# Performance work log

Hardware: AMD Instinct MI355X
Metric: run time of the kernel (lower is better)

The kernel has to match this reference:

```python
import jax, jax.numpy as jnp
import numpy as np
from math import sqrt

B, S, D_MODEL = 2, 2048, 1024
H = 16
ADIM = D_MODEL // H  # 64
K_REL = 16
N_PEMB = 2 * K_REL + 1  # 33, bidirectional rel-pos vocabulary


def setup_inputs() -> dict:
    key = jax.random.key(0)
    ks = jax.random.split(key, 8)
    sc = 0.02
    return {
        "iQ": jax.random.normal(ks[0], (B, S, D_MODEL), jnp.float32),
        "iK": jax.random.normal(ks[1], (B, S, D_MODEL), jnp.float32),
        "iV": jax.random.normal(ks[2], (B, S, D_MODEL), jnp.float32),
        "Wq": jax.random.normal(ks[3], (D_MODEL, D_MODEL), jnp.float32) * sc,
        "Wk": jax.random.normal(ks[4], (D_MODEL, D_MODEL), jnp.float32) * sc,
        "Wv": jax.random.normal(ks[5], (D_MODEL, D_MODEL), jnp.float32) * sc,
        "Wo": jax.random.normal(ks[6], (D_MODEL, D_MODEL), jnp.float32) * sc,
        "rel_pemb": jax.random.normal(ks[7], (N_PEMB, ADIM), jnp.float32) * sc,
    }


def reference(iQ, iK, iV, Wq, Wk, Wv, Wo, rel_pemb):
    b, nq, _ = iQ.shape
    seql = iK.shape[1]
    # projections -> [b, h, len, d]
    q = (iQ @ Wq).reshape(b, nq, H, ADIM).transpose(0, 2, 1, 3)
    k = (iK @ Wk).reshape(b, seql, H, ADIM).transpose(0, 2, 1, 3)
    v = (iV @ Wv).reshape(b, seql, H, ADIM).transpose(0, 2, 1, 3)
    # content scores: [b, h, nq, seql]
    scores = jnp.einsum("bhqd,bhsd->bhqs", q, k)
    # relative position bias: rel[i, j] = clamp(j - i, -K, K) + K
    pos = jnp.arange(seql)
    rel = jnp.clip(pos[None, :] - pos[:, None], -K_REL, K_REL) + K_REL
    rel = rel[seql - nq:, :]  # narrow to query rows: [nq, seql]
    e = rel_pemb[rel]  # [nq, seql, d]
    scores = scores + jnp.einsum("bhqd,qsd->bhqs", q, e)
    scores = scores / sqrt(ADIM)
    attn = jax.nn.softmax(scores, axis=-1)
    ctx = jnp.einsum("bhqs,bhsd->bqhd", attn, v).reshape(b, nq, H * ADIM)
    return ctx @ Wo
```

## Files before the change

kernel.cpp:

```cpp
#include <hip/hip_runtime.h>
#include <hip/hip_bf16.h>

#define BB 2
#define S 2048
#define DM 1024
#define H 16
#define ADIM 64
#define NP 33

typedef __bf16 bf16x8 __attribute__((ext_vector_type(8)));
typedef float f32x4 __attribute__((ext_vector_type(4)));

__global__ __launch_bounds__(256) void wtrans(
    const float* __restrict__ W0, const float* __restrict__ W1,
    const float* __restrict__ W2, __bf16* __restrict__ T0,
    __bf16* __restrict__ T1, __bf16* __restrict__ T2) {
  const float* W; __bf16* T;
  switch (blockIdx.z) {
    case 0: W = W0; T = T0; break;
    case 1: W = W1; T = T1; break;
    default: W = W2; T = T2; break;
  }
  __shared__ __bf16 tile[64][65];
  int j = threadIdx.x & 63, i0 = threadIdx.x >> 6;
  int n0 = blockIdx.x * 64, k0 = blockIdx.y * 64;
#pragma unroll
  for (int p = 0; p < 16; ++p) {
    int i = i0 + p * 4;
    tile[i][j] = (__bf16)W[(size_t)(k0 + i) * DM + n0 + j];
  }
  __syncthreads();
#pragma unroll
  for (int p = 0; p < 16; ++p) {
    int i = i0 + p * 4;
    T[(size_t)(n0 + i) * DM + k0 + j] = tile[j][i];
  }
}

#define LDK 40
template <bool A_FP32, typename CT>
__device__ __forceinline__ void gemm_body(const void* __restrict__ Av,
                                          const __bf16* __restrict__ BT,
                                          CT* __restrict__ C, int mode) {
  __shared__ __bf16 As[128 * LDK];
  __shared__ __bf16 Bs[128 * LDK];
  int t = threadIdx.x;
  int w = t >> 6, lane = t & 63, l15 = lane & 15, quad = lane >> 4;
  int wm = w >> 1, wn = w & 1;
  int m0 = blockIdx.y * 128, n0 = blockIdx.x * 128;
  f32x4 acc[4][4] = {};
  int lr = t >> 2;
  int lk = (t & 3) * 8;
  for (int k0 = 0; k0 < DM; k0 += 32) {
#pragma unroll
    for (int rr = 0; rr < 2; ++rr) {
      int row = rr * 64 + lr;
      if constexpr (A_FP32) {
        const float* src = (const float*)Av + (size_t)(m0 + row) * DM + k0 + lk;
        float4 a0 = *(const float4*)src;
        float4 a1 = *(const float4*)(src + 4);
        bf16x8 v;
        v[0] = (__bf16)a0.x; v[1] = (__bf16)a0.y;
        v[2] = (__bf16)a0.z; v[3] = (__bf16)a0.w;
        v[4] = (__bf16)a1.x; v[5] = (__bf16)a1.y;
        v[6] = (__bf16)a1.z; v[7] = (__bf16)a1.w;
        *(bf16x8*)&As[row * LDK + lk] = v;
      } else {
        *(bf16x8*)&As[row * LDK + lk] =
            *(const bf16x8*)((const __bf16*)Av + (size_t)(m0 + row) * DM + k0 + lk);
      }
      *(bf16x8*)&Bs[row * LDK + lk] =
          *(const bf16x8*)&BT[(size_t)(n0 + row) * DM + k0 + lk];
    }
    __syncthreads();
    bf16x8 af[4], bfr[4];
#pragma unroll
    for (int mi = 0; mi < 4; ++mi)
      af[mi] = *(const bf16x8*)&As[(wm * 64 + mi * 16 + l15) * LDK + quad * 8];
#pragma unroll
    for (int ni = 0; ni < 4; ++ni)
      bfr[ni] = *(const bf16x8*)&Bs[(wn * 64 + ni * 16 + l15) * LDK + quad * 8];
#pragma unroll
    for (int mi = 0; mi < 4; ++mi)
#pragma unroll
      for (int ni = 0; ni < 4; ++ni)
        acc[mi][ni] = __builtin_amdgcn_mfma_f32_16x16x32_bf16(
            af[mi], bfr[ni], acc[mi][ni], 0, 0, 0);
    __syncthreads();
  }
#pragma unroll
  for (int mi = 0; mi < 4; ++mi)
#pragma unroll
    for (int ni = 0; ni < 4; ++ni)
#pragma unroll
      for (int r = 0; r < 4; ++r) {
        int row = m0 + wm * 64 + mi * 16 + quad * 4 + r;
        int col = n0 + wn * 64 + ni * 16 + l15;
        CT v = (CT)acc[mi][ni][r];
        if (mode == 0) {
          C[(size_t)row * DM + col] = v;
        } else {
          int b = row >> 11, s = row & (S - 1);
          int h = col >> 6, d = col & (ADIM - 1);
          if (mode == 1)
            C[((size_t)(b * H + h) * S + s) * ADIM + d] = v;
          else
            C[((size_t)(b * H + h) * ADIM + d) * S + s] = v;
        }
      }
}

__global__ __launch_bounds__(256) void proj3(
    const float* __restrict__ iQ, const float* __restrict__ iK,
    const float* __restrict__ iV, const __bf16* __restrict__ WqT,
    const __bf16* __restrict__ WkT, const __bf16* __restrict__ WvT,
    __bf16* __restrict__ Qw, __bf16* __restrict__ Kw,
    __bf16* __restrict__ Vt) {
  const float* A; const __bf16* B; __bf16* C; int mode;
  switch (blockIdx.z) {
    case 0: A = iQ; B = WqT; C = Qw; mode = 1; break;
    case 1: A = iK; B = WkT; C = Kw; mode = 1; break;
    default: A = iV; B = WvT; C = Vt; mode = 2; break;
  }
  gemm_body<true, __bf16>(A, B, C, mode);
}

__global__ __launch_bounds__(256) void gemm_final(
    const __bf16* __restrict__ ctx, const __bf16* __restrict__ WoT,
    float* __restrict__ out) {
  gemm_body<false, float>(ctx, WoT, out, 0);
}

#define AST 72
__global__ __launch_bounds__(256) void attn_flash(
    const __bf16* __restrict__ Qw, const __bf16* __restrict__ Kw,
    const __bf16* __restrict__ Vt, const float* __restrict__ pemb,
    __bf16* __restrict__ ctx) {
  int bh = blockIdx.y, b = bh >> 4, h = bh & 15;
  int q0 = blockIdx.x * 64;
  int t = threadIdx.x, w = t >> 6, lane = t & 63, l15 = lane & 15,
      quad = lane >> 4;
  const __bf16* Qh = Qw + (size_t)bh * S * ADIM;
  const __bf16* Kh = Kw + (size_t)bh * S * ADIM;
  const __bf16* Vh = Vt + (size_t)bh * ADIM * S;

  __shared__ __align__(16) char smem[36352];
  __bf16* Ks = (__bf16*)smem;
  __bf16* Vs = (__bf16*)(smem + 9216);
  float* pband = (float*)(smem + 18432);
  __bf16* pbufw = (__bf16*)(smem + 27136 + w * 2304);
  __bf16* peb = (__bf16*)smem;

  for (int i = t; i < 48 * 64; i += 256) {
    int r = i >> 6, d = i & 63;
    peb[r * AST + d] = (r < NP) ? (__bf16)pemb[i] : (__bf16)0.f;
  }

  int qa = q0 + w * 16 + l15;
  bf16x8 qf0 = *(const bf16x8*)&Qh[(size_t)qa * ADIM + quad * 8];
  bf16x8 qf1 = *(const bf16x8*)&Qh[(size_t)qa * ADIM + 32 + quad * 8];
  __syncthreads();

  {
    f32x4 pc[3] = {};
#pragma unroll
    for (int ni = 0; ni < 3; ++ni) {
      bf16x8 b0 = *(const bf16x8*)&peb[(ni * 16 + l15) * AST + quad * 8];
      bf16x8 b1 = *(const bf16x8*)&peb[(ni * 16 + l15) * AST + 32 + quad * 8];
      pc[ni] = __builtin_amdgcn_mfma_f32_16x16x32_bf16(qf0, b0, pc[ni], 0, 0, 0);
      pc[ni] = __builtin_amdgcn_mfma_f32_16x16x32_bf16(qf1, b1, pc[ni], 0, 0, 0);
    }
#pragma unroll
    for (int ni = 0; ni < 3; ++ni)
#pragma unroll
      for (int r = 0; r < 4; ++r) {
        int col = ni * 16 + l15;
        if (col < NP) pband[(w * 16 + quad * 4 + r) * 34 + col] = pc[ni][r];
      }
  }
  __syncthreads();

  int qc = q0 + w * 16 + quad * 4;
  int lrow = w * 16 + quad * 4;
  int qw0 = q0 + w * 16;
  float lsum[4] = {0.f, 0.f, 0.f, 0.f};
  f32x4 o[4] = {};

  float blo[4], bhi[4];
#pragma unroll
  for (int r = 0; r < 4; ++r) {
    blo[r] = __expf(pband[(lrow + r) * 34 + 0] * 0.125f);
    bhi[r] = __expf(pband[(lrow + r) * 34 + 32] * 0.125f);
  }

  int srow = t >> 3;
  int scol = (t & 7) * 8;
  bf16x8 k0r = *(const bf16x8*)&Kh[(size_t)srow * ADIM + scol];
  bf16x8 k1r = *(const bf16x8*)&Kh[(size_t)(32 + srow) * ADIM + scol];
  bf16x8 v0r = *(const bf16x8*)&Vh[(size_t)srow * S + scol];
  bf16x8 v1r = *(const bf16x8*)&Vh[(size_t)(32 + srow) * S + scol];

  for (int s0 = 0; s0 < S; s0 += 64) {
    __syncthreads();
    *(bf16x8*)&Ks[srow * AST + scol] = k0r;
    *(bf16x8*)&Ks[(32 + srow) * AST + scol] = k1r;
    *(bf16x8*)&Vs[srow * AST + scol] = v0r;
    *(bf16x8*)&Vs[(32 + srow) * AST + scol] = v1r;
    int sn = s0 + 64;
    if (sn < S) {
      k0r = *(const bf16x8*)&Kh[(size_t)(sn + srow) * ADIM + scol];
      k1r = *(const bf16x8*)&Kh[(size_t)(sn + 32 + srow) * ADIM + scol];
      v0r = *(const bf16x8*)&Vh[(size_t)srow * S + sn + scol];
      v1r = *(const bf16x8*)&Vh[(size_t)(32 + srow) * S + sn + scol];
    }
    __syncthreads();

    f32x4 c[4];
#pragma unroll
    for (int j = 0; j < 4; ++j) {
      f32x4 cj = {};
      bf16x8 kb0 = *(const bf16x8*)&Ks[(j * 16 + l15) * AST + quad * 8];
      bf16x8 kb1 = *(const bf16x8*)&Ks[(j * 16 + l15) * AST + 32 + quad * 8];
      cj = __builtin_amdgcn_mfma_f32_16x16x32_bf16(qf0, kb0, cj, 0, 0, 0);
      cj = __builtin_amdgcn_mfma_f32_16x16x32_bf16(qf1, kb1, cj, 0, 0, 0);
      c[j] = cj;
    }

    float pv[4][4];
    bool below = (s0 + 79 <= qw0);
    bool above = (s0 >= qw0 + 31);
    if (below || above) {
#pragma unroll
      for (int j = 0; j < 4; ++j)
#pragma unroll
        for (int r = 0; r < 4; ++r) {
          float f = below ? blo[r] : bhi[r];
          float e = __expf(c[j][r] * 0.125f) * f;
          lsum[r] += e;
          pv[j][r] = e;
        }
    } else {
#pragma unroll
      for (int j = 0; j < 4; ++j)
#pragma unroll
        for (int r = 0; r < 4; ++r) {
          int qg = qc + r;
          int sg = s0 + j * 16 + l15;
          int i0 = sg - qg; i0 = i0 < -16 ? -16 : (i0 > 16 ? 16 : i0); i0 += 16;
          float e = __expf((c[j][r] + pband[(lrow + r) * 34 + i0]) * 0.125f);
          lsum[r] += e;
          pv[j][r] = e;
        }
    }

#pragma unroll
    for (int j = 0; j < 4; ++j)
#pragma unroll
      for (int r = 0; r < 4; ++r)
        pbufw[(quad * 4 + r) * AST + j * 16 + l15] = (__bf16)pv[j][r];
    bf16x8 pa0 = *(const bf16x8*)&pbufw[l15 * AST + quad * 8];
    bf16x8 pa1 = *(const bf16x8*)&pbufw[l15 * AST + 32 + quad * 8];

#pragma unroll
    for (int nt = 0; nt < 4; ++nt) {
      bf16x8 vb0 = *(const bf16x8*)&Vs[(nt * 16 + l15) * AST + quad * 8];
      bf16x8 vb1 = *(const bf16x8*)&Vs[(nt * 16 + l15) * AST + 32 + quad * 8];
      o[nt] = __builtin_amdgcn_mfma_f32_16x16x32_bf16(pa0, vb0, o[nt], 0, 0, 0);
      o[nt] = __builtin_amdgcn_mfma_f32_16x16x32_bf16(pa1, vb1, o[nt], 0, 0, 0);
    }
  }

#pragma unroll
  for (int r = 0; r < 4; ++r) {
#pragma unroll
    for (int mm = 1; mm < 16; mm <<= 1) lsum[r] += __shfl_xor(lsum[r], mm, 64);
  }
#pragma unroll
  for (int nt = 0; nt < 4; ++nt)
#pragma unroll
    for (int r = 0; r < 4; ++r) {
      int qg = qc + r;
      int d = nt * 16 + l15;
      ctx[(size_t)(b * S + qg) * DM + h * ADIM + d] =
          (__bf16)(o[nt][r] / lsum[r]);
    }
}

extern "C" void kernel_launch(void* const* d_in, const int* in_sizes, int n_in,
                              void* d_out, int out_size, void* d_ws,
                              size_t ws_size, hipStream_t stream) {
  bool sizes_ok =
      (n_in == 8 && in_sizes[0] == BB * S * DM && in_sizes[1] == BB * S * DM &&
       in_sizes[2] == BB * S * DM && in_sizes[3] == DM * DM &&
       in_sizes[4] == DM * DM && in_sizes[5] == DM * DM &&
       in_sizes[6] == DM * DM && in_sizes[7] == NP * ADIM &&
       out_size == BB * S * DM);
  if (!sizes_ok) return;
  if (ws_size < 33ull * 1024 * 1024) return;

  const float* iQ = (const float*)d_in[0];
  const float* iK = (const float*)d_in[1];
  const float* iV = (const float*)d_in[2];
  const float* Wq = (const float*)d_in[3];
  const float* Wk = (const float*)d_in[4];
  const float* Wv = (const float*)d_in[5];
  const float* Wo = (const float*)d_in[6];
  const float* pemb = (const float*)d_in[7];

  char* w = (char*)d_ws;
  const size_t MB = 1024 * 1024;
  __bf16* Qw  = (__bf16*)(w + 0 * MB);
  __bf16* Kw  = (__bf16*)(w + 8 * MB);
  __bf16* Vt  = (__bf16*)(w + 16 * MB);
  __bf16* ctx = (__bf16*)(w + 24 * MB);
  __bf16* WqT = (__bf16*)(w + 24 * MB);
  __bf16* WkT = (__bf16*)(w + 26 * MB);
  __bf16* WvT = (__bf16*)(w + 28 * MB);
  __bf16* WoT = (__bf16*)(w + 0 * MB);

  wtrans<<<dim3(16, 16, 3), 256, 0, stream>>>(Wq, Wk, Wv, WqT, WkT, WvT);
  proj3<<<dim3(8, 32, 3), 256, 0, stream>>>(iQ, iK, iV, WqT, WkT, WvT,
                                            Qw, Kw, Vt);
  attn_flash<<<dim3(S / 64, BB * H), 256, 0, stream>>>(Qw, Kw, Vt, pemb, ctx);
  wtrans<<<dim3(16, 16, 1), 256, 0, stream>>>(Wo, Wo, Wo, WoT, WoT, WoT);
  gemm_final<<<dim3(8, 32), 256, 0, stream>>>(ctx, WoT, (float*)d_out);
}
```

Before: 270.5 us.

## Shrink GEMM M-tile to 64, double-buffer K tile, read V fragments from global

The projection and output GEMMs now use a 64-row M tile with twice as many blocks, meant to raise occupancy and fill more CUs. In attention, V is no longer staged through shared memory: MFMA B fragments are loaded directly from the transposed V in global memory. K is ping-ponged between two LDS buffers so one barrier per iteration is removed. The cost is lower data reuse per GEMM block and uncoalesced, latency-exposed global V loads inside the inner loop.

```diff
diff --git a/kernel.cpp b/kernel.cpp
--- a/kernel.cpp
+++ b/kernel.cpp
@@ -38,22 +38,23 @@
 }
 
 #define LDK 40
-template <bool A_FP32, typename CT>
+template <int RB, bool A_FP32, typename CT>
 __device__ __forceinline__ void gemm_body(const void* __restrict__ Av,
                                           const __bf16* __restrict__ BT,
                                           CT* __restrict__ C, int mode) {
-  __shared__ __bf16 As[128 * LDK];
+  constexpr int MI = RB / 32;
+  __shared__ __bf16 As[RB * LDK];
   __shared__ __bf16 Bs[128 * LDK];
   int t = threadIdx.x;
   int w = t >> 6, lane = t & 63, l15 = lane & 15, quad = lane >> 4;
   int wm = w >> 1, wn = w & 1;
-  int m0 = blockIdx.y * 128, n0 = blockIdx.x * 128;
-  f32x4 acc[4][4] = {};
+  int m0 = blockIdx.y * RB, n0 = blockIdx.x * 128;
+  f32x4 acc[MI][4] = {};
   int lr = t >> 2;
   int lk = (t & 3) * 8;
   for (int k0 = 0; k0 < DM; k0 += 32) {
 #pragma unroll
-    for (int rr = 0; rr < 2; ++rr) {
+    for (int rr = 0; rr < RB / 64; ++rr) {
       int row = rr * 64 + lr;
       if constexpr (A_FP32) {
         const float* src = (const float*)Av + (size_t)(m0 + row) * DM + k0 + lk;
@@ -69,19 +70,23 @@
         *(bf16x8*)&As[row * LDK + lk] =
             *(const bf16x8*)((const __bf16*)Av + (size_t)(m0 + row) * DM + k0 + lk);
       }
+    }
+#pragma unroll
+    for (int rr = 0; rr < 2; ++rr) {
+      int row = rr * 64 + lr;
       *(bf16x8*)&Bs[row * LDK + lk] =
           *(const bf16x8*)&BT[(size_t)(n0 + row) * DM + k0 + lk];
     }
     __syncthreads();
-    bf16x8 af[4], bfr[4];
-#pragma unroll
-    for (int mi = 0; mi < 4; ++mi)
-      af[mi] = *(const bf16x8*)&As[(wm * 64 + mi * 16 + l15) * LDK + quad * 8];
+    bf16x8 af[MI], bfr[4];
+#pragma unroll
+    for (int mi = 0; mi < MI; ++mi)
+      af[mi] = *(const bf16x8*)&As[(wm * (RB / 2) + mi * 16 + l15) * LDK + quad * 8];
 #pragma unroll
     for (int ni = 0; ni < 4; ++ni)
       bfr[ni] = *(const bf16x8*)&Bs[(wn * 64 + ni * 16 + l15) * LDK + quad * 8];
 #pragma unroll
-    for (int mi = 0; mi < 4; ++mi)
+    for (int mi = 0; mi < MI; ++mi)
 #pragma unroll
       for (int ni = 0; ni < 4; ++ni)
         acc[mi][ni] = __builtin_amdgcn_mfma_f32_16x16x32_bf16(
@@ -89,12 +94,12 @@
     __syncthreads();
   }
 #pragma unroll
-  for (int mi = 0; mi < 4; ++mi)
+  for (int mi = 0; mi < MI; ++mi)
 #pragma unroll
     for (int ni = 0; ni < 4; ++ni)
 #pragma unroll
       for (int r = 0; r < 4; ++r) {
-        int row = m0 + wm * 64 + mi * 16 + quad * 4 + r;
+        int row = m0 + wm * (RB / 2) + mi * 16 + quad * 4 + r;
         int col = n0 + wn * 64 + ni * 16 + l15;
         CT v = (CT)acc[mi][ni][r];
         if (mode == 0) {
@@ -122,13 +127,13 @@
     case 1: A = iK; B = WkT; C = Kw; mode = 1; break;
     default: A = iV; B = WvT; C = Vt; mode = 2; break;
   }
-  gemm_body<true, __bf16>(A, B, C, mode);
+  gemm_body<64, true, __bf16>(A, B, C, mode);
 }
 
 __global__ __launch_bounds__(256) void gemm_final(
     const __bf16* __restrict__ ctx, const __bf16* __restrict__ WoT,
     float* __restrict__ out) {
-  gemm_body<false, float>(ctx, WoT, out, 0);
+  gemm_body<64, false, float>(ctx, WoT, out, 0);
 }
 
 #define AST 72
@@ -145,8 +150,8 @@
   const __bf16* Vh = Vt + (size_t)bh * ADIM * S;
 
   __shared__ __align__(16) char smem[36352];
-  __bf16* Ks = (__bf16*)smem;
-  __bf16* Vs = (__bf16*)(smem + 9216);
+  __bf16* KsA = (__bf16*)smem;
+  __bf16* KsB = (__bf16*)(smem + 9216);
   float* pband = (float*)(smem + 18432);
   __bf16* pbufw = (__bf16*)(smem + 27136 + w * 2304);
   __bf16* peb = (__bf16*)smem;
@@ -197,21 +202,15 @@
   int scol = (t & 7) * 8;
   bf16x8 k0r = *(const bf16x8*)&Kh[(size_t)srow * ADIM + scol];
   bf16x8 k1r = *(const bf16x8*)&Kh[(size_t)(32 + srow) * ADIM + scol];
-  bf16x8 v0r = *(const bf16x8*)&Vh[(size_t)srow * S + scol];
-  bf16x8 v1r = *(const bf16x8*)&Vh[(size_t)(32 + srow) * S + scol];
 
   for (int s0 = 0; s0 < S; s0 += 64) {
-    __syncthreads();
-    *(bf16x8*)&Ks[srow * AST + scol] = k0r;
-    *(bf16x8*)&Ks[(32 + srow) * AST + scol] = k1r;
-    *(bf16x8*)&Vs[srow * AST + scol] = v0r;
-    *(bf16x8*)&Vs[(32 + srow) * AST + scol] = v1r;
+    __bf16* cur = ((s0 >> 6) & 1) ? KsB : KsA;
+    *(bf16x8*)&cur[srow * AST + scol] = k0r;
+    *(bf16x8*)&cur[(32 + srow) * AST + scol] = k1r;
     int sn = s0 + 64;
     if (sn < S) {
       k0r = *(const bf16x8*)&Kh[(size_t)(sn + srow) * ADIM + scol];
       k1r = *(const bf16x8*)&Kh[(size_t)(sn + 32 + srow) * ADIM + scol];
-      v0r = *(const bf16x8*)&Vh[(size_t)srow * S + sn + scol];
-      v1r = *(const bf16x8*)&Vh[(size_t)(32 + srow) * S + sn + scol];
     }
     __syncthreads();
 
@@ -219,8 +218,8 @@
 #pragma unroll
     for (int j = 0; j < 4; ++j) {
       f32x4 cj = {};
-      bf16x8 kb0 = *(const bf16x8*)&Ks[(j * 16 + l15) * AST + quad * 8];
-      bf16x8 kb1 = *(const bf16x8*)&Ks[(j * 16 + l15) * AST + 32 + quad * 8];
+      bf16x8 kb0 = *(const bf16x8*)&cur[(j * 16 + l15) * AST + quad * 8];
+      bf16x8 kb1 = *(const bf16x8*)&cur[(j * 16 + l15) * AST + 32 + quad * 8];
       cj = __builtin_amdgcn_mfma_f32_16x16x32_bf16(qf0, kb0, cj, 0, 0, 0);
       cj = __builtin_amdgcn_mfma_f32_16x16x32_bf16(qf1, kb1, cj, 0, 0, 0);
       c[j] = cj;
@@ -263,8 +262,8 @@
 
 #pragma unroll
     for (int nt = 0; nt < 4; ++nt) {
-      bf16x8 vb0 = *(const bf16x8*)&Vs[(nt * 16 + l15) * AST + quad * 8];
-      bf16x8 vb1 = *(const bf16x8*)&Vs[(nt * 16 + l15) * AST + 32 + quad * 8];
+      bf16x8 vb0 = *(const bf16x8*)&Vh[(size_t)(nt * 16 + l15) * S + s0 + quad * 8];
+      bf16x8 vb1 = *(const bf16x8*)&Vh[(size_t)(nt * 16 + l15) * S + s0 + 32 + quad * 8];
       o[nt] = __builtin_amdgcn_mfma_f32_16x16x32_bf16(pa0, vb0, o[nt], 0, 0, 0);
       o[nt] = __builtin_amdgcn_mfma_f32_16x16x32_bf16(pa1, vb1, o[nt], 0, 0, 0);
     }
@@ -319,9 +318,9 @@
   __bf16* WoT = (__bf16*)(w + 0 * MB);
 
   wtrans<<<dim3(16, 16, 3), 256, 0, stream>>>(Wq, Wk, Wv, WqT, WkT, WvT);
-  proj3<<<dim3(8, 32, 3), 256, 0, stream>>>(iQ, iK, iV, WqT, WkT, WvT,
+  proj3<<<dim3(8, 64, 3), 256, 0, stream>>>(iQ, iK, iV, WqT, WkT, WvT,
                                             Qw, Kw, Vt);
   attn_flash<<<dim3(S / 64, BB * H), 256, 0, stream>>>(Qw, Kw, Vt, pemb, ctx);
   wtrans<<<dim3(16, 16, 1), 256, 0, stream>>>(Wo, Wo, Wo, WoT, WoT, WoT);
-  gemm_final<<<dim3(8, 32), 256, 0, stream>>>(ctx, WoT, (float*)d_out);
-}
+  gemm_final<<<dim3(8, 64), 256, 0, stream>>>(ctx, WoT, (float*)d_out);
+}
```

Measured after the change: 346.1 us. 28.0% more time.
